# Kernel tuning notes

Measured on AMD Instinct MI355X. Metric: run time of the kernel, lower is better.

The kernel has to match this reference:

```python
import jax, jax.numpy as jnp
import numpy as np

NUM_REL = 6
EMBED_DIM = 128
B, N = 8, 1024


def _relation_type(dx, dy):
    # Faithful to _get_relation_type's if/elif chain (order matters).
    return jnp.select(
        [dy > 0.5,
         dy < -0.5,
         dx < -0.5,
         dx > 0.5,
         (jnp.abs(dx) < 0.3) & (jnp.abs(dy) < 0.3)],
        [0, 1, 2, 3, 4],
        5,
    )


def setup_inputs() -> dict:
    key = jax.random.key(0)
    k1, k2, k3, k4 = jax.random.split(key, 4)
    symbols = jax.random.normal(k1, (B, N, EMBED_DIM), dtype=jnp.float32)
    positions = jax.random.normal(k2, (B, N, 2), dtype=jnp.float32)
    # 6 Linear(embed_dim, embed_dim) layers, stacked: W [6, D, D] (torch layout: y = x @ W.T + b)
    bound = 1.0 / np.sqrt(EMBED_DIM)
    W = jax.random.uniform(k3, (NUM_REL, EMBED_DIM, EMBED_DIM), dtype=jnp.float32,
                           minval=-bound, maxval=bound)
    b = jax.random.uniform(k4, (NUM_REL, EMBED_DIM), dtype=jnp.float32,
                           minval=-bound, maxval=bound)
    return {"symbols": symbols, "positions": positions, "W": W, "b": b}


def reference(symbols, positions, W, b):
    Bn, Nn, D = symbols.shape
    # dx[b,i,j] = pos[b,j,0] - pos[b,i,0]; dy likewise (source i -> target j)
    dx = positions[:, None, :, 0] - positions[:, :, None, 0]  # [B, i, j]
    dy = positions[:, None, :, 1] - positions[:, :, None, 1]
    rel = _relation_type(dx, dy)  # [B, i, j] in {0..5}

    # Per-type transform of every source symbol: T[r,b,i,:] = symbols[b,i] @ W[r].T + b[r]
    T = jnp.einsum('bid,red->rbie', symbols, W) + b[:, None, None, :]  # [6, B, N, D]

    # One-hot relation mask with i != j excluded; scatter-add into targets j.
    not_diag = ~jnp.eye(Nn, dtype=bool)  # [i, j]
    mask = (rel[None] == jnp.arange(NUM_REL)[:, None, None, None]) & not_diag  # [6, B, i, j]
    agg = jnp.einsum('rbij,rbie->bje', mask.astype(symbols.dtype), T)  # [B, N, D]
    return symbols + agg
```

## Files before the change

kernel.cpp:

```cpp
#include <hip/hip_runtime.h>
#include <stdint.h>


typedef __attribute__((ext_vector_type(8))) short bf16x8;
typedef __attribute__((ext_vector_type(4))) float f32x4;
union U4B { uint4 u; bf16x8 b; };

#if defined(__has_builtin)
#  if __has_builtin(__builtin_amdgcn_global_load_lds)
#    define HAVE_GLL 1
#  endif
#  if __has_builtin(__builtin_amdgcn_mul_u24)
#    define OH_MUL24 1
#  endif
#endif

__device__ __forceinline__ uint16_t f2bf(float f) {
    union { float f; uint32_t u; } v; v.f = f;
    uint32_t u = v.u;
    uint32_t r = (u + 0x7FFFu + ((u >> 16) & 1u)) >> 16;
    return (uint16_t)r;
}

__global__ __launch_bounds__(256)
void prep_kernel(const float* __restrict__ X, const float* __restrict__ W,
                 uint16_t* __restrict__ symT, uint16_t* __restrict__ WtB) {
    const int blk = blockIdx.x, tid = threadIdx.x;
    if (blk < 256) {
        __shared__ float T[64 * 65];
        const int b = blk & 7, z = blk >> 3, it = z & 15, et = z >> 4;
        const int i0 = it * 64, e0 = et * 64;
        const float4* Xf = (const float4*)X;
#pragma unroll
        for (int s = 0; s < 4; ++s) {
            int il = s * 16 + (tid >> 4), e4 = tid & 15;
            float4 v = Xf[((size_t)b << 15) + (size_t)((i0 + il) << 5) + (e0 >> 2) + e4];
            T[il * 65 + e4 * 4 + 0] = v.x;
            T[il * 65 + e4 * 4 + 1] = v.y;
            T[il * 65 + e4 * 4 + 2] = v.z;
            T[il * 65 + e4 * 4 + 3] = v.w;
        }
        __syncthreads();
#pragma unroll
        for (int s = 0; s < 4; ++s) {
            int el = s * 16 + (tid >> 4), il4 = tid & 15;
            uint16_t h0 = f2bf(T[(il4 * 4 + 0) * 65 + el]);
            uint16_t h1 = f2bf(T[(il4 * 4 + 1) * 65 + el]);
            uint16_t h2 = f2bf(T[(il4 * 4 + 2) * 65 + el]);
            uint16_t h3 = f2bf(T[(il4 * 4 + 3) * 65 + el]);
            uint2 pk = { (uint32_t)h0 | ((uint32_t)h1 << 16),
                         (uint32_t)h2 | ((uint32_t)h3 << 16) };
            *(uint2*)&symT[((size_t)b << 17) + ((size_t)(e0 + el) << 10) + i0 + il4 * 4] = pk;
        }
    } else {
        int g = (blk - 256) * 256 + tid;
        float4 v = ((const float4*)W)[g];
        int r = g >> 12, rem = g & 4095, ep = rem >> 5, e4 = rem & 31;
        int kb = r * 4 + (e4 >> 3);
        int kc = (e4 & 7) * 4;
        uint16_t h0 = f2bf(v.x), h1 = f2bf(v.y), h2 = f2bf(v.z), h3 = f2bf(v.w);
        uint2 pk = { (uint32_t)h0 | ((uint32_t)h1 << 16),
                     (uint32_t)h2 | ((uint32_t)h3 << 16) };
        *(uint2*)&WtB[((size_t)(kb * 128 + ep)) * 32 + kc] = pk;
    }
}

#define SP 776

__global__ __launch_bounds__(512)
void fused_kernel(const float* __restrict__ sym, const float* __restrict__ pos,
                  const uint16_t* __restrict__ symT, const uint16_t* __restrict__ WtB,
                  const float* __restrict__ bias, float* __restrict__ out) {
    __shared__ __align__(16) char smem[81920];
    uint16_t* symTS   = (uint16_t*)smem;
    float2*   posS    = (float2*)(smem + 32768);
    uint16_t* SA      = (uint16_t*)smem;
    float*    partial = (float*)(smem + 24832);
    uint32_t* rel32   = (uint32_t*)(smem + 65536);

    const int blk = blockIdx.x;
    const int b = blk & 7, jt = blk >> 3, j0 = jt * 16;
    const int tid = threadIdx.x;
    const int w = tid >> 6, lane = tid & 63, m = lane & 15, q = lane >> 4;

    const uint16_t* symTb = symT + ((size_t)b << 17);

    int goff[4];
#pragma unroll
    for (int s = 0; s < 4; ++s) {
        int c16 = s * 512 + tid;
        int e = c16 >> 4, sg = (c16 & 15) ^ (e & 15);
        goff[s] = (e << 10) + sg * 8;
    }
    const int lwb = w * 1024;

    auto issue_chunk = [&](int cidx, int bufsel) {
#ifdef HAVE_GLL
#pragma unroll
        for (int s = 0; s < 4; ++s) {
            const uint16_t* gp = symTb + goff[s] + cidx * 128;
            char* lp = smem + bufsel * 32768 + s * 8192 + lwb;
            typedef const __attribute__((address_space(1))) uint32_t gu32;
            typedef __attribute__((address_space(3))) uint32_t lu32;
            __builtin_amdgcn_global_load_lds((gu32*)gp, (lu32*)lp, 16, 0, 0);
        }
#else
#pragma unroll
        for (int s = 0; s < 4; ++s) {
            uint4 v = *(const uint4*)(symTb + goff[s] + cidx * 128);
            *(uint4*)(smem + bufsel * 32768 + (s * 512 + tid) * 16) = v;
        }
#endif
    };

    issue_chunk(0, 0);

    const float2* pos2 = (const float2*)pos + ((size_t)b << 10);
    posS[tid] = pos2[tid];
    posS[tid + 512] = pos2[tid + 512];
    __syncthreads();

    {
        const int mm = tid & 15, grp = tid >> 4;
        const int j = j0 + mm;
        const float2 pj = posS[j];
        uint32_t* dst = &rel32[mm * 256];
        const int sw = mm * 2;
#pragma unroll
        for (int s = 0; s < 8; ++s) {
            uint32_t word = 0;
#pragma unroll
            for (int qq = 0; qq < 4; ++qq) {
                int i = grp * 32 + s * 4 + qq;
                float2 pi = posS[i];
                float dx = pj.x - pi.x, dy = pj.y - pi.y;
                int r = (dy > 0.5f) ? 0
                      : (dy < -0.5f) ? 1
                      : (dx < -0.5f) ? 2
                      : (dx > 0.5f)  ? 3
                      : (fabsf(dx) < 0.3f && fabsf(dy) < 0.3f) ? 4
                      : 5;
                uint32_t oh = (i == j) ? 0u : (1u << r);
                word |= oh << (8 * qq);
            }
            dst[(grp * 8 + s) ^ sw] = word;
        }
    }
    __syncthreads();

    f32x4 acc[6];
#pragma unroll
    for (int r = 0; r < 6; ++r) acc[r] = (f32x4){0.f, 0.f, 0.f, 0.f};

    const int E = w * 16 + m;
    const int esw = E & 15;
    const int csw = m * 2;

    for (int c = 0; c < 8; ++c) {
        if (c < 7) issue_chunk(c + 1, (c + 1) & 1);
        const uint16_t* bt = symTS + ((c & 1) << 14) + E * 128;
        const uint32_t* crow = &rel32[m * 256 + c * 32];
#pragma unroll
        for (int ks = 0; ks < 4; ++ks) {
            U4B bfr;
            bfr.u = *(const uint4*)(bt + ((((ks << 2) + q) ^ esw) << 3));
            uint2 cw = *(const uint2*)&crow[(((ks << 3) + (q << 1)) ^ csw)];
            uint32_t hx01 = __builtin_amdgcn_perm(cw.x, cw.x, 0x01010000u) & 0x00FF00FFu;
            uint32_t hx23 = __builtin_amdgcn_perm(cw.x, cw.x, 0x03030202u) & 0x00FF00FFu;
            uint32_t hy01 = __builtin_amdgcn_perm(cw.y, cw.y, 0x01010000u) & 0x00FF00FFu;
            uint32_t hy23 = __builtin_amdgcn_perm(cw.y, cw.y, 0x03030202u) & 0x00FF00FFu;
#pragma unroll
            for (int r = 0; r < 6; ++r) {
                const uint32_t rm = 0x00010001u << r;
                U4B a;
#ifdef OH_MUL24
                const uint32_t mc = 0x3F80u >> r;
                a.u.x = (uint32_t)__builtin_amdgcn_mul_u24((int)(hx01 & rm), (int)mc);
                a.u.y = (uint32_t)__builtin_amdgcn_mul_u24((int)(hx23 & rm), (int)mc);
                a.u.z = (uint32_t)__builtin_amdgcn_mul_u24((int)(hy01 & rm), (int)mc);
                a.u.w = (uint32_t)__builtin_amdgcn_mul_u24((int)(hy23 & rm), (int)mc);
#else
                uint32_t g2;
                g2 = hx01 & rm; a.u.x = (g2 << (14 - r)) - (g2 << (7 - r));
                g2 = hx23 & rm; a.u.y = (g2 << (14 - r)) - (g2 << (7 - r));
                g2 = hy01 & rm; a.u.z = (g2 << (14 - r)) - (g2 << (7 - r));
                g2 = hy23 & rm; a.u.w = (g2 << (14 - r)) - (g2 << (7 - r));
#endif
                acc[r] = __builtin_amdgcn_mfma_f32_16x16x32_bf16(a.b, bfr.b, acc[r], 0, 0, 0);
            }
        }
        __syncthreads();
    }

#pragma unroll
    for (int r = 0; r < 6; ++r)
#pragma unroll
        for (int reg = 0; reg < 4; ++reg)
            SA[(q * 4 + reg) * SP + r * 128 + w * 16 + m] = f2bf(acc[r][reg]);
    __syncthreads();

    {
        const int g = w >> 1, h = w & 1;
        f32x4 c2[4];
#pragma unroll
        for (int nf = 0; nf < 4; ++nf) c2[nf] = (f32x4){0.f, 0.f, 0.f, 0.f};
#pragma unroll
        for (int kf = 0; kf < 6; ++kf) {
            U4B af;
            af.u = *(const uint4*)&SA[m * SP + g * 192 + kf * 32 + q * 8];
            const int kb = g * 6 + kf;
#pragma unroll
            for (int nf = 0; nf < 4; ++nf) {
                U4B bw;
                bw.u = *(const uint4*)&WtB[((size_t)(kb * 128 + h * 64 + nf * 16 + m)) * 32 + q * 8];
                c2[nf] = __builtin_amdgcn_mfma_f32_16x16x32_bf16(af.b, bw.b, c2[nf], 0, 0, 0);
            }
        }
#pragma unroll
        for (int nf = 0; nf < 4; ++nf)
#pragma unroll
            for (int reg = 0; reg < 4; ++reg)
                partial[g * 2112 + (q * 4 + reg) * 132 + h * 64 + nf * 16 + m] = c2[nf][reg];
    }
    __syncthreads();

    {
        const int j = tid >> 5, t = tid & 31, e0 = t << 2;
        const uint32_t* row = &rel32[j * 256 + t * 8];
        uint32_t s0 = 0, s1 = 0, s2 = 0, s3 = 0, s4 = 0, s5 = 0;
#pragma unroll
        for (int k = 0; k < 8; ++k) {
            uint32_t wd = row[k];
            s0 += wd & 0x01010101u;        s1 += (wd >> 1) & 0x01010101u;
            s2 += (wd >> 2) & 0x01010101u; s3 += (wd >> 3) & 0x01010101u;
            s4 += (wd >> 4) & 0x01010101u; s5 += (wd >> 5) & 0x01010101u;
        }
        int cnt[6];
        cnt[0] = (int)((s0 * 0x01010101u) >> 24);
        cnt[1] = (int)((s1 * 0x01010101u) >> 24);
        cnt[2] = (int)((s2 * 0x01010101u) >> 24);
        cnt[3] = (int)((s3 * 0x01010101u) >> 24);
        cnt[4] = (int)((s4 * 0x01010101u) >> 24);
        cnt[5] = (int)((s5 * 0x01010101u) >> 24);
#pragma unroll
        for (int off = 1; off < 32; off <<= 1)
#pragma unroll
            for (int r = 0; r < 6; ++r)
                cnt[r] += __shfl_xor(cnt[r], off, 64);

        float4 a4 = {0.f, 0.f, 0.f, 0.f};
#pragma unroll
        for (int g4 = 0; g4 < 4; ++g4) {
            float4 u = *(const float4*)&partial[g4 * 2112 + j * 132 + e0];
            a4.x += u.x; a4.y += u.y; a4.z += u.z; a4.w += u.w;
        }
#pragma unroll
        for (int r = 0; r < 6; ++r) {
            float cf = (float)cnt[r];
            float4 bb = *(const float4*)&bias[r * 128 + e0];
            a4.x += cf * bb.x; a4.y += cf * bb.y; a4.z += cf * bb.z; a4.w += cf * bb.w;
        }
        size_t o = ((size_t)(b * 1024 + j0 + j) << 7) + e0;
        float4 sv = *(const float4*)&sym[o];
        float4 ov = { sv.x + a4.x, sv.y + a4.y, sv.z + a4.z, sv.w + a4.w };
        *(float4*)&out[o] = ov;
    }
}

extern "C" void kernel_launch(void* const* d_in, const int* in_sizes, int n_in,
                              void* d_out, int out_size, void* d_ws, size_t ws_size,
                              hipStream_t stream) {
    const float* symbols   = (const float*)d_in[0];
    const float* positions = (const float*)d_in[1];
    const float* W         = (const float*)d_in[2];
    const float* bias      = (const float*)d_in[3];
    float* out             = (float*)d_out;

    char* ws = (char*)d_ws;
    uint16_t* symT = (uint16_t*)ws;
    uint16_t* WtB  = (uint16_t*)(ws + 2097152);

    prep_kernel<<<352, 256, 0, stream>>>(symbols, W, symT, WtB);
    fused_kernel<<<512, 512, 0, stream>>>(symbols, positions, symT, WtB, bias, out);
}
```

Baseline: 92.21 us.

## Derive sixth relation aggregate from column sums to drop one MFMA accumulator

Adds a prep stage that computes per-batch column sums of bf16-rounded symbols. The main loop then accumulates only five relation types, and the sixth is recovered as total sum minus self minus the other five. This cuts the one-hot generation and MFMA work in the hot loop by a sixth. The second GEMM is also restructured so each wave does a full 24-step K reduction for its own 16 output columns, which removes the cross-wave partial-sum reduction through shared memory. The subtraction-based sixth term may add rounding error, and the prep kernel does extra serial reduction work.

```diff
diff --git a/kernel.cpp b/kernel.cpp
--- a/kernel.cpp
+++ b/kernel.cpp
@@ -21,13 +21,17 @@
     uint32_t r = (u + 0x7FFFu + ((u >> 16) & 1u)) >> 16;
     return (uint16_t)r;
 }
+__device__ __forceinline__ float bfv(uint32_t bits) {
+    union { uint32_t u; float f; } v; v.u = bits; return v.f;
+}
 
 __global__ __launch_bounds__(256)
 void prep_kernel(const float* __restrict__ X, const float* __restrict__ W,
-                 uint16_t* __restrict__ symT, uint16_t* __restrict__ WtB) {
+                 uint16_t* __restrict__ symT, uint16_t* __restrict__ WtB,
+                 float* __restrict__ allsumF) {
     const int blk = blockIdx.x, tid = threadIdx.x;
+    __shared__ float T[64 * 65];
     if (blk < 256) {
-        __shared__ float T[64 * 65];
         const int b = blk & 7, z = blk >> 3, it = z & 15, et = z >> 4;
         const int i0 = it * 64, e0 = et * 64;
         const float4* Xf = (const float4*)X;
@@ -52,7 +56,7 @@
                          (uint32_t)h2 | ((uint32_t)h3 << 16) };
             *(uint2*)&symT[((size_t)b << 17) + ((size_t)(e0 + el) << 10) + i0 + il4 * 4] = pk;
         }
-    } else {
+    } else if (blk < 352) {
         int g = (blk - 256) * 256 + tid;
         float4 v = ((const float4*)W)[g];
         int r = g >> 12, rem = g & 4095, ep = rem >> 5, e4 = rem & 31;
@@ -62,6 +66,19 @@
         uint2 pk = { (uint32_t)h0 | ((uint32_t)h1 << 16),
                      (uint32_t)h2 | ((uint32_t)h3 << 16) };
         *(uint2*)&WtB[((size_t)(kb * 128 + ep)) * 32 + kc] = pk;
+    } else {
+        const int b = blk - 352;
+        const int e = tid & 127, ih = tid >> 7;
+        const float* Xb = X + ((size_t)b << 17);
+        float s = 0.f;
+#pragma unroll 4
+        for (int i = ih * 512; i < ih * 512 + 512; ++i) {
+            float v = Xb[((size_t)i << 7) + e];
+            s += bfv((uint32_t)f2bf(v) << 16);
+        }
+        if (ih == 1) T[e] = s;
+        __syncthreads();
+        if (ih == 0) allsumF[b * 128 + e] = s + T[e];
     }
 }
 
@@ -70,13 +87,13 @@
 __global__ __launch_bounds__(512)
 void fused_kernel(const float* __restrict__ sym, const float* __restrict__ pos,
                   const uint16_t* __restrict__ symT, const uint16_t* __restrict__ WtB,
-                  const float* __restrict__ bias, float* __restrict__ out) {
+                  const float* __restrict__ bias, const float* __restrict__ allsumF,
+                  float* __restrict__ out) {
     __shared__ __align__(16) char smem[81920];
-    uint16_t* symTS   = (uint16_t*)smem;
-    float2*   posS    = (float2*)(smem + 32768);
-    uint16_t* SA      = (uint16_t*)smem;
-    float*    partial = (float*)(smem + 24832);
-    uint32_t* rel32   = (uint32_t*)(smem + 65536);
+    uint16_t* SA     = (uint16_t*)smem;
+    float*    ctile  = (float*)(smem + 24832);
+    float2*   posS   = (float2*)(smem + 32768);
+    uint32_t* rel32  = (uint32_t*)(smem + 65536);
 
     const int blk = blockIdx.x;
     const int b = blk & 7, jt = blk >> 3, j0 = jt * 16;
@@ -85,21 +102,14 @@
 
     const uint16_t* symTb = symT + ((size_t)b << 17);
 
-    int goff[4];
-#pragma unroll
-    for (int s = 0; s < 4; ++s) {
-        int c16 = s * 512 + tid;
-        int e = c16 >> 4, sg = (c16 & 15) ^ (e & 15);
-        goff[s] = (e << 10) + sg * 8;
-    }
-    const int lwb = w * 1024;
-
     auto issue_chunk = [&](int cidx, int bufsel) {
 #ifdef HAVE_GLL
 #pragma unroll
         for (int s = 0; s < 4; ++s) {
-            const uint16_t* gp = symTb + goff[s] + cidx * 128;
-            char* lp = smem + bufsel * 32768 + s * 8192 + lwb;
+            int c16 = s * 512 + tid;
+            int e = c16 >> 4, sg = (c16 & 15) ^ (e & 15);
+            const uint16_t* gp = symTb + (e << 10) + cidx * 128 + sg * 8;
+            char* lp = smem + bufsel * 32768 + s * 8192 + w * 1024;
             typedef const __attribute__((address_space(1))) uint32_t gu32;
             typedef __attribute__((address_space(3))) uint32_t lu32;
             __builtin_amdgcn_global_load_lds((gu32*)gp, (lu32*)lp, 16, 0, 0);
@@ -107,8 +117,10 @@
 #else
 #pragma unroll
         for (int s = 0; s < 4; ++s) {
-            uint4 v = *(const uint4*)(symTb + goff[s] + cidx * 128);
-            *(uint4*)(smem + bufsel * 32768 + (s * 512 + tid) * 16) = v;
+            int c16 = s * 512 + tid;
+            int e = c16 >> 4, sg = (c16 & 15) ^ (e & 15);
+            uint4 v = *(const uint4*)(symTb + (e << 10) + cidx * 128 + sg * 8);
+            *(uint4*)(smem + bufsel * 32768 + c16 * 16) = v;
         }
 #endif
     };
@@ -148,29 +160,28 @@
     }
     __syncthreads();
 
-    f32x4 acc[6];
-#pragma unroll
-    for (int r = 0; r < 6; ++r) acc[r] = (f32x4){0.f, 0.f, 0.f, 0.f};
+    f32x4 acc[5];
+#pragma unroll
+    for (int r = 0; r < 5; ++r) acc[r] = (f32x4){0.f, 0.f, 0.f, 0.f};
 
     const int E = w * 16 + m;
-    const int esw = E & 15;
     const int csw = m * 2;
 
     for (int c = 0; c < 8; ++c) {
         if (c < 7) issue_chunk(c + 1, (c + 1) & 1);
-        const uint16_t* bt = symTS + ((c & 1) << 14) + E * 128;
+        const uint16_t* bt = (const uint16_t*)(smem + ((c & 1) << 15)) + E * 128;
         const uint32_t* crow = &rel32[m * 256 + c * 32];
 #pragma unroll
         for (int ks = 0; ks < 4; ++ks) {
             U4B bfr;
-            bfr.u = *(const uint4*)(bt + ((((ks << 2) + q) ^ esw) << 3));
+            bfr.u = *(const uint4*)(bt + ((((ks << 2) + q) ^ m) << 3));
             uint2 cw = *(const uint2*)&crow[(((ks << 3) + (q << 1)) ^ csw)];
             uint32_t hx01 = __builtin_amdgcn_perm(cw.x, cw.x, 0x01010000u) & 0x00FF00FFu;
             uint32_t hx23 = __builtin_amdgcn_perm(cw.x, cw.x, 0x03030202u) & 0x00FF00FFu;
             uint32_t hy01 = __builtin_amdgcn_perm(cw.y, cw.y, 0x01010000u) & 0x00FF00FFu;
             uint32_t hy23 = __builtin_amdgcn_perm(cw.y, cw.y, 0x03030202u) & 0x00FF00FFu;
 #pragma unroll
-            for (int r = 0; r < 6; ++r) {
+            for (int r = 0; r < 5; ++r) {
                 const uint32_t rm = 0x00010001u << r;
                 U4B a;
 #ifdef OH_MUL24
@@ -192,45 +203,53 @@
         __syncthreads();
     }
 
-#pragma unroll
-    for (int r = 0; r < 6; ++r)
+    {
+        uint2 sjv = *(const uint2*)(symTb + ((size_t)E << 10) + j0 + q * 4);
+        float asum = allsumF[b * 128 + E];
+        float sj[4];
+        sj[0] = bfv(sjv.x << 16);
+        sj[1] = bfv(sjv.x & 0xFFFF0000u);
+        sj[2] = bfv(sjv.y << 16);
+        sj[3] = bfv(sjv.y & 0xFFFF0000u);
+#pragma unroll
+        for (int reg = 0; reg < 4; ++reg) {
+            const int row = (q * 4 + reg) * SP;
+            float s01 = acc[0][reg] + acc[1][reg];
+            float s23 = acc[2][reg] + acc[3][reg];
+            float ssum = s01 + s23 + acc[4][reg];
+#pragma unroll
+            for (int r = 0; r < 5; ++r)
+                SA[row + r * 128 + E] = f2bf(acc[r][reg]);
+            SA[row + 5 * 128 + E] = f2bf(asum - sj[reg] - ssum);
+        }
+    }
+    __syncthreads();
+
+    {
+        f32x4 c2 = {0.f, 0.f, 0.f, 0.f};
+#pragma unroll
+        for (int kb = 0; kb < 24; ++kb) {
+            U4B af, bw;
+            af.u = *(const uint4*)&SA[m * SP + kb * 32 + q * 8];
+            bw.u = *(const uint4*)&WtB[(((size_t)(kb * 128 + E)) << 5) + q * 8];
+            c2 = __builtin_amdgcn_mfma_f32_16x16x32_bf16(af.b, bw.b, c2, 0, 0, 0);
+        }
 #pragma unroll
         for (int reg = 0; reg < 4; ++reg)
-            SA[(q * 4 + reg) * SP + r * 128 + w * 16 + m] = f2bf(acc[r][reg]);
+            ctile[(q * 4 + reg) * 132 + E] = c2[reg];
+    }
     __syncthreads();
 
     {
-        const int g = w >> 1, h = w & 1;
-        f32x4 c2[4];
-#pragma unroll
-        for (int nf = 0; nf < 4; ++nf) c2[nf] = (f32x4){0.f, 0.f, 0.f, 0.f};
-#pragma unroll
-        for (int kf = 0; kf < 6; ++kf) {
-            U4B af;
-            af.u = *(const uint4*)&SA[m * SP + g * 192 + kf * 32 + q * 8];
-            const int kb = g * 6 + kf;
-#pragma unroll
-            for (int nf = 0; nf < 4; ++nf) {
-                U4B bw;
-                bw.u = *(const uint4*)&WtB[((size_t)(kb * 128 + h * 64 + nf * 16 + m)) * 32 + q * 8];
-                c2[nf] = __builtin_amdgcn_mfma_f32_16x16x32_bf16(af.b, bw.b, c2[nf], 0, 0, 0);
-            }
-        }
-#pragma unroll
-        for (int nf = 0; nf < 4; ++nf)
-#pragma unroll
-            for (int reg = 0; reg < 4; ++reg)
-                partial[g * 2112 + (q * 4 + reg) * 132 + h * 64 + nf * 16 + m] = c2[nf][reg];
-    }
-    __syncthreads();
-
-    {
-        const int j = tid >> 5, t = tid & 31, e0 = t << 2;
-        const uint32_t* row = &rel32[j * 256 + t * 8];
+        const int j = tid >> 5, t = tid & 31, e0 = t * 4;
+        const uint32_t* row = &rel32[j * 256];
+        uint4 ra = *(const uint4*)&row[t * 8];
+        uint4 rb = *(const uint4*)&row[t * 8 + 4];
         uint32_t s0 = 0, s1 = 0, s2 = 0, s3 = 0, s4 = 0, s5 = 0;
+        uint32_t wds[8] = { ra.x, ra.y, ra.z, ra.w, rb.x, rb.y, rb.z, rb.w };
 #pragma unroll
         for (int k = 0; k < 8; ++k) {
-            uint32_t wd = row[k];
+            uint32_t wd = wds[k];
             s0 += wd & 0x01010101u;        s1 += (wd >> 1) & 0x01010101u;
             s2 += (wd >> 2) & 0x01010101u; s3 += (wd >> 3) & 0x01010101u;
             s4 += (wd >> 4) & 0x01010101u; s5 += (wd >> 5) & 0x01010101u;
@@ -248,12 +267,7 @@
             for (int r = 0; r < 6; ++r)
                 cnt[r] += __shfl_xor(cnt[r], off, 64);
 
-        float4 a4 = {0.f, 0.f, 0.f, 0.f};
-#pragma unroll
-        for (int g4 = 0; g4 < 4; ++g4) {
-            float4 u = *(const float4*)&partial[g4 * 2112 + j * 132 + e0];
-            a4.x += u.x; a4.y += u.y; a4.z += u.z; a4.w += u.w;
-        }
+        float4 a4 = *(const float4*)&ctile[j * 132 + e0];
 #pragma unroll
         for (int r = 0; r < 6; ++r) {
             float cf = (float)cnt[r];
@@ -277,9 +291,11 @@
     float* out             = (float*)d_out;
 
     char* ws = (char*)d_ws;
-    uint16_t* symT = (uint16_t*)ws;
-    uint16_t* WtB  = (uint16_t*)(ws + 2097152);
-
-    prep_kernel<<<352, 256, 0, stream>>>(symbols, W, symT, WtB);
-    fused_kernel<<<512, 512, 0, stream>>>(symbols, positions, symT, WtB, bias, out);
-}
+    uint16_t* symT    = (uint16_t*)ws;
+    uint16_t* WtB     = (uint16_t*)(ws + 2097152);
+    float*    allsumF = (float*)(ws + 2293760);
+
+    prep_kernel<<<360, 256, 0, stream>>>(symbols, W, symT, WtB, allsumF);
+    fused_kernel<<<512, 512, 0, stream>>>(symbols, positions, symT, WtB, bias,
+                                          allsumF, out);
+}
```

After: 108.9 us. 18.1% more time.

## Split relation accumulation into two passes of three accumulators each

Applied to the files above, without the earlier changes.

The per-relation MFMA accumulation now runs in two passes, each holding three accumulator tiles instead of six, to lower register pressure. The second pass streams the symbol chunks from global memory again into a single LDS buffer, with a barrier before each compute step, so it gets no prefetch overlap. The precomputed global offsets are also recomputed inside the load lambda. This trades doubled symbol traffic and a serialized second pass for fewer live VGPRs and possibly higher occupancy.

```diff
diff --git a/kernel.cpp b/kernel.cpp
--- a/kernel.cpp
+++ b/kernel.cpp
@@ -72,10 +72,9 @@
                   const uint16_t* __restrict__ symT, const uint16_t* __restrict__ WtB,
                   const float* __restrict__ bias, float* __restrict__ out) {
     __shared__ __align__(16) char smem[81920];
-    uint16_t* symTS   = (uint16_t*)smem;
-    float2*   posS    = (float2*)(smem + 32768);
     uint16_t* SA      = (uint16_t*)smem;
     float*    partial = (float*)(smem + 24832);
+    float2*   posS    = (float2*)(smem + 32768);
     uint32_t* rel32   = (uint32_t*)(smem + 65536);
 
     const int blk = blockIdx.x;
@@ -85,21 +84,14 @@
 
     const uint16_t* symTb = symT + ((size_t)b << 17);
 
-    int goff[4];
-#pragma unroll
-    for (int s = 0; s < 4; ++s) {
-        int c16 = s * 512 + tid;
-        int e = c16 >> 4, sg = (c16 & 15) ^ (e & 15);
-        goff[s] = (e << 10) + sg * 8;
-    }
-    const int lwb = w * 1024;
-
     auto issue_chunk = [&](int cidx, int bufsel) {
 #ifdef HAVE_GLL
 #pragma unroll
         for (int s = 0; s < 4; ++s) {
-            const uint16_t* gp = symTb + goff[s] + cidx * 128;
-            char* lp = smem + bufsel * 32768 + s * 8192 + lwb;
+            int c16 = s * 512 + tid;
+            int e = c16 >> 4, sg = (c16 & 15) ^ (e & 15);
+            const uint16_t* gp = symTb + (e << 10) + cidx * 128 + sg * 8;
+            char* lp = smem + bufsel * 32768 + s * 8192 + w * 1024;
             typedef const __attribute__((address_space(1))) uint32_t gu32;
             typedef __attribute__((address_space(3))) uint32_t lu32;
             __builtin_amdgcn_global_load_lds((gu32*)gp, (lu32*)lp, 16, 0, 0);
@@ -107,8 +99,10 @@
 #else
 #pragma unroll
         for (int s = 0; s < 4; ++s) {
-            uint4 v = *(const uint4*)(symTb + goff[s] + cidx * 128);
-            *(uint4*)(smem + bufsel * 32768 + (s * 512 + tid) * 16) = v;
+            int c16 = s * 512 + tid;
+            int e = c16 >> 4, sg = (c16 & 15) ^ (e & 15);
+            uint4 v = *(const uint4*)(symTb + (e << 10) + cidx * 128 + sg * 8);
+            *(uint4*)(smem + bufsel * 32768 + c16 * 16) = v;
         }
 #endif
     };
@@ -148,29 +142,24 @@
     }
     __syncthreads();
 
-    f32x4 acc[6];
-#pragma unroll
-    for (int r = 0; r < 6; ++r) acc[r] = (f32x4){0.f, 0.f, 0.f, 0.f};
-
     const int E = w * 16 + m;
-    const int esw = E & 15;
     const int csw = m * 2;
 
-    for (int c = 0; c < 8; ++c) {
-        if (c < 7) issue_chunk(c + 1, (c + 1) & 1);
-        const uint16_t* bt = symTS + ((c & 1) << 14) + E * 128;
-        const uint32_t* crow = &rel32[m * 256 + c * 32];
+    auto compute_chunk = [&](int d, int buf, int rbase, f32x4* acc) {
+        const uint16_t* bt = (const uint16_t*)(smem + (buf << 15)) + E * 128;
+        const uint32_t* crow = &rel32[m * 256 + d * 32];
 #pragma unroll
         for (int ks = 0; ks < 4; ++ks) {
             U4B bfr;
-            bfr.u = *(const uint4*)(bt + ((((ks << 2) + q) ^ esw) << 3));
+            bfr.u = *(const uint4*)(bt + ((((ks << 2) + q) ^ m) << 3));
             uint2 cw = *(const uint2*)&crow[(((ks << 3) + (q << 1)) ^ csw)];
             uint32_t hx01 = __builtin_amdgcn_perm(cw.x, cw.x, 0x01010000u) & 0x00FF00FFu;
             uint32_t hx23 = __builtin_amdgcn_perm(cw.x, cw.x, 0x03030202u) & 0x00FF00FFu;
             uint32_t hy01 = __builtin_amdgcn_perm(cw.y, cw.y, 0x01010000u) & 0x00FF00FFu;
             uint32_t hy23 = __builtin_amdgcn_perm(cw.y, cw.y, 0x03030202u) & 0x00FF00FFu;
 #pragma unroll
-            for (int r = 0; r < 6; ++r) {
+            for (int rr = 0; rr < 3; ++rr) {
+                const int r = rbase + rr;
                 const uint32_t rm = 0x00010001u << r;
                 U4B a;
 #ifdef OH_MUL24
@@ -186,17 +175,39 @@
                 g2 = hy01 & rm; a.u.z = (g2 << (14 - r)) - (g2 << (7 - r));
                 g2 = hy23 & rm; a.u.w = (g2 << (14 - r)) - (g2 << (7 - r));
 #endif
-                acc[r] = __builtin_amdgcn_mfma_f32_16x16x32_bf16(a.b, bfr.b, acc[r], 0, 0, 0);
+                acc[rr] = __builtin_amdgcn_mfma_f32_16x16x32_bf16(a.b, bfr.b, acc[rr], 0, 0, 0);
             }
         }
-        __syncthreads();
-    }
-
-#pragma unroll
-    for (int r = 0; r < 6; ++r)
+    };
+
+    f32x4 acc[3];
+
+#pragma unroll
+    for (int rr = 0; rr < 3; ++rr) acc[rr] = (f32x4){0.f, 0.f, 0.f, 0.f};
+    for (int c = 0; c < 8; ++c) {
+        if (c < 7) issue_chunk(c + 1, (c + 1) & 1);
+        compute_chunk(c, c & 1, 0, acc);
+        __syncthreads();
+    }
+#pragma unroll
+    for (int rr = 0; rr < 3; ++rr)
 #pragma unroll
         for (int reg = 0; reg < 4; ++reg)
-            SA[(q * 4 + reg) * SP + r * 128 + w * 16 + m] = f2bf(acc[r][reg]);
+            SA[(q * 4 + reg) * SP + rr * 128 + E] = f2bf(acc[rr][reg]);
+
+#pragma unroll
+    for (int rr = 0; rr < 3; ++rr) acc[rr] = (f32x4){0.f, 0.f, 0.f, 0.f};
+    for (int c = 0; c < 8; ++c) {
+        issue_chunk(c, 1);
+        __syncthreads();
+        compute_chunk(c, 1, 3, acc);
+        __syncthreads();
+    }
+#pragma unroll
+    for (int rr = 0; rr < 3; ++rr)
+#pragma unroll
+        for (int reg = 0; reg < 4; ++reg)
+            SA[(q * 4 + reg) * SP + (rr + 3) * 128 + E] = f2bf(acc[rr][reg]);
     __syncthreads();
 
     {
```

New measurement: 96.93 us. 5.1% more time.
